# Kernel tuning notes

Measured on AMD Instinct MI355X. Metric: run time of the kernel, lower is better.

The kernel has to match this reference:

```python
import jax, jax.numpy as jnp
import numpy as np

ALPHA = 0.05
MAX_ITER = 200
TOL = 0.01
N = 64
M = 1
BATCH = 262144


def setup_inputs() -> dict:
    key = jax.random.key(0)
    pred_cost = jax.random.normal(key, (BATCH, N), dtype=jnp.float32)
    # constraint data (fixed buffers, match init_kwargs)
    A = np.ones((M, N), dtype=np.float32)
    b = np.full((M,), 32.0, dtype=np.float32)
    lb = np.zeros((N,), dtype=np.float32)
    ub = np.ones((N,), dtype=np.float32)
    # SVD-based pseudoinverse factors for equality projection
    U, s, VT = np.linalg.svd(A, full_matrices=False)
    s_inv = np.where(s >= 1e-6, 1.0 / s, 0.0).astype(np.float32)
    return {
        "pred_cost": pred_cost,
        "A": jnp.asarray(A),
        "b": jnp.asarray(b),
        "lb": jnp.asarray(lb),
        "ub": jnp.asarray(ub),
        "V": jnp.asarray(VT.T.astype(np.float32)),   # (n, m)
        "UT": jnp.asarray(U.T.astype(np.float32)),   # (m, m)
        "s_inv": jnp.asarray(s_inv),                 # (m,)
    }


def _project_box(z, lb, ub):
    return jnp.clip(z, lb, ub)


def _project_equality(w, A, b, V, UT, s_inv):
    # w: (B, n). residual r = A w^T - b, correction = V diag(s_inv) U^T r
    r = w @ A.T - b                      # (B, m)
    corr = ((r @ UT.T) * s_inv) @ V.T    # (B, n)
    return w - corr


def _dys_step(z, cost, A, b, lb, ub, V, UT, s_inv):
    x = _project_box(z, lb, ub)
    grad = cost + ALPHA * x              # grad of regularized objective
    y = _project_equality(2.0 * x - z - ALPHA * grad, A, b, V, UT, s_inv)
    return z - x + y


def _run_to_convergence(cost, A, b, lb, ub, V, UT, s_inv):
    lb_safe = jnp.where(jnp.isfinite(lb), lb, 0.0)
    ub_safe = jnp.where(jnp.isfinite(ub), ub, 1.0)
    z0 = jax.random.uniform(jax.random.key(1), cost.shape, dtype=cost.dtype)
    z0 = z0 * (ub_safe - lb_safe) + lb_safe

    def cond(state):
        i, z, diff = state
        return jnp.logical_and(i < MAX_ITER, diff > TOL)

    def body(state):
        i, z, _ = state
        z_new = _dys_step(z, cost, A, b, lb, ub, V, UT, s_inv)
        diff = jnp.max(jnp.linalg.norm(z_new - z, axis=1))
        return (i + 1, z_new, diff)

    _, z, _ = jax.lax.while_loop(cond, body, (jnp.int32(0), z0, jnp.float32(1e30)))
    return z


def reference(pred_cost, A, b, lb, ub, V, UT, s_inv):
    cost = pred_cost  # minimize=True
    # no-grad fixed-point iterations
    z = jax.lax.stop_gradient(
        _run_to_convergence(jax.lax.stop_gradient(cost), A, b, lb, ub, V, UT, s_inv)
    )
    # training branch: one differentiable DYS step (JFB), then box projection
    z = _dys_step(z, cost, A, b, lb, ub, V, UT, s_inv)
    sol = _project_box(z, lb, ub)
    return sol
```

## Files before the change

kernel.cpp:

```cpp
#include <hip/hip_runtime.h>
#include <cstdint>


#ifndef JAX_PARTITIONABLE
#define JAX_PARTITIONABLE 1
#endif

#define BATCHN 262144
#define MAXIT  200

#define PROBE_ROWS 8192
#define RPW_P  4
#define PROBE_WAVES_P (PROBE_ROWS / RPW_P)

#define NWAVES_A 16384

#define RPW_D  16
#define NWAVES_D (BATCHN / RPW_D)

#define K1 0.9975f
#define K2 1.9975f

typedef float v2f __attribute__((ext_vector_type(2)));

__device__ __forceinline__ void tf2x32(uint32_t x0, uint32_t x1,
                                       uint32_t& o0, uint32_t& o1) {
  const uint32_t k0 = 0u, k1 = 1u;
  const uint32_t k2 = 0x1BD11BDAu ^ k0 ^ k1;
  x0 += k0; x1 += k1;
#define TFR(r) { x0 += x1; x1 = (x1 << (r)) | (x1 >> (32 - (r))); x1 ^= x0; }
  TFR(13) TFR(15) TFR(26) TFR(6)   x0 += k1; x1 += k2 + 1u;
  TFR(17) TFR(29) TFR(16) TFR(24)  x0 += k2; x1 += k0 + 2u;
  TFR(13) TFR(15) TFR(26) TFR(6)   x0 += k0; x1 += k1 + 3u;
  TFR(17) TFR(29) TFR(16) TFR(24)  x0 += k1; x1 += k2 + 4u;
  TFR(13) TFR(15) TFR(26) TFR(6)   x0 += k2; x1 += k0 + 5u;
#undef TFR
  o0 = x0; o1 = x1;
}

__device__ __forceinline__ float z0_at(uint32_t f) {
  uint32_t b;
#if JAX_PARTITIONABLE
  uint32_t o0, o1;
  tf2x32(0u, f, o0, o1);
  b = o0 ^ o1;
#else
  const uint32_t H = 8388608u;
  uint32_t lo = (f < H) ? f : (f - H);
  uint32_t o0, o1;
  tf2x32(lo, lo + H, o0, o1);
  b = (f < H) ? o0 : o1;
#endif
  return __uint_as_float((b >> 9) | 0x3f800000u) - 1.0f;
}

template <int CTRL>
__device__ __forceinline__ float dpp_add(float v) {
  int s = __builtin_amdgcn_mov_dpp(__float_as_int(v), CTRL, 0xF, 0xF, true);
  return v + __int_as_float(s);
}

__device__ __forceinline__ float reduce4(float v) {
  v = dpp_add<0xB1>(v);
  v = dpp_add<0x4E>(v);
  return v;
}

template <int CTRL>
__device__ __forceinline__ v2f dpp_addv(v2f v) {
  int sx = __builtin_amdgcn_mov_dpp(__float_as_int(v.x), CTRL, 0xF, 0xF, true);
  int sy = __builtin_amdgcn_mov_dpp(__float_as_int(v.y), CTRL, 0xF, 0xF, true);
  v2f s;
  s.x = __int_as_float(sx);
  s.y = __int_as_float(sy);
  return v + s;
}

__device__ __forceinline__ v2f reduce16v(v2f v) {
  v = dpp_addv<0xB1>(v);
  v = dpp_addv<0x4E>(v);
  v = dpp_addv<0x124>(v);
  v = dpp_addv<0x128>(v);
  return v;
}

__global__ __launch_bounds__(256, 4) void dys_probe(
    const float* __restrict__ cost, int* __restrict__ Tsample) {
  const int lane = threadIdx.x & 63;
  const int wid  = threadIdx.x >> 6;
  const int gw = blockIdx.x * 4 + wid;
  const int base = (gw * RPW_P + (lane >> 4)) * 64 + (lane & 15) * 4;

  const v2f K1p = {K1, K1};
  const float4 cq = *(const float4*)(cost + base);
  v2f nc0, nc1;
  nc0.x = -cq.x; nc0.y = -cq.y; nc1.x = -cq.z; nc1.y = -cq.w;

  const float z0 = z0_at((uint32_t)(base + 0));
  const float z1 = z0_at((uint32_t)(base + 1));
  const float z2 = z0_at((uint32_t)(base + 2));
  const float z3 = z0_at((uint32_t)(base + 3));
  v2f U0, U1;
  U0.x = 20.0f * z0; U0.y = 20.0f * z1;
  U1.x = 20.0f * z2; U1.y = 20.0f * z3;

  v2f zc;
  zc.x = (z0 + z1) + (z2 + z3);
  zc.y = (cq.x + cq.y) + (cq.z + cq.w);
  zc = reduce16v(zc);
  float R   = __builtin_fmaf(0.05f, zc.y, zc.x);
  const float Snc = -zc.y;
  float SU  = 20.0f * zc.x;
  float CC = 0.0f;

  int ib = MAXIT;
  for (int i = 1; i <= MAXIT; ++i) {
    const float Ch = CC + 20.0f;
    v2f sp, q2v = {0.0f, 0.0f};
    v2f m2, un2, d2;
    m2.x = __builtin_amdgcn_fmed3f(U0.x, CC, Ch);
    m2.y = __builtin_amdgcn_fmed3f(U0.y, CC, Ch);
    sp = m2;
    un2 = __builtin_elementwise_fma(K1p, m2, nc0);
    d2 = un2 - U0;
    q2v = __builtin_elementwise_fma(d2, d2, q2v);
    U0 = un2;
    m2.x = __builtin_amdgcn_fmed3f(U1.x, CC, Ch);
    m2.y = __builtin_amdgcn_fmed3f(U1.y, CC, Ch);
    sp += m2;
    un2 = __builtin_elementwise_fma(K1p, m2, nc1);
    d2 = un2 - U1;
    q2v = __builtin_elementwise_fma(d2, d2, q2v);
    U1 = un2;

    v2f red;
    red.x = sp.x + sp.y;
    red.y = q2v.x + q2v.y;
    red = reduce16v(red);
    const float s_ = red.x;
    const float q2 = red.y;

    const float SUn = __builtin_fmaf(K1, s_, Snc);
    const float q1 = SUn - SU;
    SU = SUn;

    const float Sx = 0.05f * __builtin_fmaf(-64.0f, CC, s_);
    const float t_ = __builtin_fmaf(K2, Sx, -R);
    const float corr20 = __builtin_fmaf(t_, 0.3125f, -10.0f);
    R = (R - Sx) + 32.0f;
    const float CCn = __builtin_fmaf(K1, CC, corr20);
    const float dCC = CCn - CC;
    CC = CCn;
    const float a_ = __builtin_fmaf(64.0f, dCC, -2.0f * q1);
    const float ds = __builtin_fmaf(dCC, a_, q2);
    if (__all(ds <= 0.04f)) { ib = i; break; }
  }

  __shared__ int ibs[4];
  if (lane == 0) ibs[wid] = ib;
  __syncthreads();
  if (threadIdx.x == 0) {
    const int m01 = ibs[0] > ibs[1] ? ibs[0] : ibs[1];
    const int m23 = ibs[2] > ibs[3] ? ibs[2] : ibs[3];
    atomicMax(Tsample, m01 > m23 ? m01 : m23);
  }
}


#define P8(X) X(0) X(1) X(2) X(3) X(4) X(5) X(6) X(7)

#define PAIRS4(X) X(0,0,1) X(1,2,3) X(2,4,5) X(3,6,7)

#define DECL_STATE(p) v2f U##p, nc##p;

#define PIN(p) asm("" : "+v"(U##p), "+v"(nc##p));

#define LOADC(k, p0, p1) { \
  const float4 cq = *(const float4*)(cost + base + 4 * (k)); \
  nc##p0.x = -cq.x; nc##p0.y = -cq.y; nc##p1.x = -cq.z; nc##p1.y = -cq.w; }

#define INITU(p) { \
  const float za = z0_at((uint32_t)(base + 2 * (p))); \
  const float zb = z0_at((uint32_t)(base + 2 * (p) + 1)); \
  U##p.x = 20.0f * za; U##p.y = 20.0f * zb; \
  r0 = __builtin_fmaf(-0.05f, nc##p.x, r0 + za); \
  r1 = __builtin_fmaf(-0.05f, nc##p.y, r1 + zb); }

#define FSTEP(p) { v2f m2; \
  m2.x = __builtin_amdgcn_fmed3f(U##p.x, CC, Ch); \
  m2.y = __builtin_amdgcn_fmed3f(U##p.y, CC, Ch); \
  if ((p) & 1) spB += m2; else spA += m2; \
  U##p = __builtin_elementwise_fma(K1p, m2, nc##p); }

#define FAST_ITER() { \
  const float Ch = CC + 20.0f; \
  v2f spA = {0.0f, 0.0f}, spB = {0.0f, 0.0f}; \
  P8(FSTEP) \
  const v2f spc = spA + spB; \
  const float s_ = reduce4(spc.x + spc.y); \
  const float Sx = 0.05f * __builtin_fmaf(-64.0f, CC, s_); \
  const float t_ = __builtin_fmaf(K2, Sx, -R); \
  const float corr20 = __builtin_fmaf(t_, 0.3125f, -10.0f); \
  R = (R - Sx) + 32.0f; \
  CC = __builtin_fmaf(K1, CC, corr20); }

#define CSTEP(p) { v2f m2; \
  m2.x = __builtin_amdgcn_fmed3f(U##p.x, CC, Ch); \
  m2.y = __builtin_amdgcn_fmed3f(U##p.y, CC, Ch); \
  if ((p) & 1) spB += m2; else spA += m2; \
  const v2f un2 = __builtin_elementwise_fma(K1p, m2, nc##p); \
  const v2f d2 = un2 - U##p; \
  q1v += d2; \
  q2v = __builtin_elementwise_fma(d2, d2, q2v); \
  U##p = un2; }

#define CHK_ITER(DS) { \
  const float Ch = CC + 20.0f; \
  v2f spA = {0.0f, 0.0f}, spB = {0.0f, 0.0f}; \
  v2f q1v = {0.0f, 0.0f}, q2v = {0.0f, 0.0f}; \
  P8(CSTEP) \
  const v2f spc = spA + spB; \
  const float s_ = reduce4(spc.x + spc.y); \
  const float Sx = 0.05f * __builtin_fmaf(-64.0f, CC, s_); \
  const float t_ = __builtin_fmaf(K2, Sx, -R); \
  const float corr20 = __builtin_fmaf(t_, 0.3125f, -10.0f); \
  R = (R - Sx) + 32.0f; \
  const float CCn = __builtin_fmaf(K1, CC, corr20); \
  const float dCC = CCn - CC; CC = CCn; \
  const float q1 = reduce4(q1v.x + q1v.y); \
  const float q2 = reduce4(q2v.x + q2v.y); \
  const float a_ = __builtin_fmaf(64.0f, dCC, -2.0f * q1); \
  DS = __builtin_fmaf(dCC, a_, q2); }

#define STZ(k, p0, p1) { float4 zq; \
  zq.x = __builtin_fmaf(0.05f, U##p0.x, -CC05); \
  zq.y = __builtin_fmaf(0.05f, U##p0.y, -CC05); \
  zq.z = __builtin_fmaf(0.05f, U##p1.x, -CC05); \
  zq.w = __builtin_fmaf(0.05f, U##p1.y, -CC05); \
  *(float4*)(zst + base + 4 * (k)) = zq; }

#define LOADZ(k, p0, p1) { \
  const float4 zq = *(const float4*)(zst + base + 4 * (k)); \
  U##p0.x = 20.0f * zq.x; U##p0.y = 20.0f * zq.y; \
  U##p1.x = 20.0f * zq.z; U##p1.y = 20.0f * zq.w; \
  r0 += zq.x + zq.y; r1 += zq.z + zq.w; }

#define RC(p) { r0 = __builtin_fmaf(-0.05f, nc##p.x, r0); \
  r1 = __builtin_fmaf(-0.05f, nc##p.y, r1); }

#define STOUT(k, p0, p1) { float4 o; \
  o.x = __builtin_amdgcn_fmed3f( \
      __builtin_fmaf(0.05f, U##p0.x, -CC05), 0.0f, 1.0f); \
  o.y = __builtin_amdgcn_fmed3f( \
      __builtin_fmaf(0.05f, U##p0.y, -CC05), 0.0f, 1.0f); \
  o.z = __builtin_amdgcn_fmed3f( \
      __builtin_fmaf(0.05f, U##p1.x, -CC05), 0.0f, 1.0f); \
  o.w = __builtin_amdgcn_fmed3f( \
      __builtin_fmaf(0.05f, U##p1.y, -CC05), 0.0f, 1.0f); \
  *(float4*)(out + base + 4 * (k)) = o; }

__global__ __attribute__((amdgpu_flat_work_group_size(256, 256),
                          amdgpu_waves_per_eu(4, 8)))
void dys_pass1(
    const float* __restrict__ cost, const int* __restrict__ Tsample,
    int* __restrict__ Tglob, int* __restrict__ TrArr,
    float* __restrict__ zst) {
  const int lane = threadIdx.x & 63;
  const int gw = blockIdx.x * 4 + (threadIdx.x >> 6);
  const int base = (gw * RPW_D + (lane >> 2)) * 64 + (lane & 3) * 16;

  const v2f K1p = {K1, K1};
  P8(DECL_STATE)
  PAIRS4(LOADC)
  float r0 = 0.0f, r1 = 0.0f;
  P8(INITU)
  P8(PIN)
  float R = reduce4(r0 + r1);
  float CC = 0.0f;

  const int Ts = *Tsample;
  const int Pn = (Ts > 2) ? (Ts - 2) : 0;

  for (int i = 0; i < Pn; ++i) FAST_ITER();

  int ib = MAXIT;
  for (int i = Pn + 1; i <= MAXIT; ++i) {
    float ds;
    CHK_ITER(ds)
    if (__all(ds <= 0.04f)) { ib = i; break; }
  }

  const float CC05 = 0.05f * CC;
  PAIRS4(STZ)
  if (lane == 0) {
    TrArr[gw] = ib;
    atomicMax(Tglob, ib);
  }
}

__global__ __attribute__((amdgpu_flat_work_group_size(256, 256),
                          amdgpu_waves_per_eu(4, 8)))
void dys_pass2(
    const float* __restrict__ cost, const int* __restrict__ Tglob,
    const int* __restrict__ TrArr, const float* __restrict__ zst,
    float* __restrict__ out) {
  const int lane = threadIdx.x & 63;
  const int gw = blockIdx.x * 4 + (threadIdx.x >> 6);
  const int base = (gw * RPW_D + (lane >> 2)) * 64 + (lane & 3) * 16;

  const v2f K1p = {K1, K1};
  P8(DECL_STATE)
  PAIRS4(LOADC)
  float r0 = 0.0f, r1 = 0.0f;
  PAIRS4(LOADZ)
  P8(RC)
  P8(PIN)
  float R = reduce4(r0 + r1);
  float CC = 0.0f;

  const int T = *Tglob;
  const int ib = TrArr[gw];

  for (int i = ib; i <= T; ++i) FAST_ITER();

  const float CC05 = 0.05f * CC;
  PAIRS4(STOUT)
}

extern "C" void kernel_launch(void* const* d_in, const int* in_sizes, int n_in,
                              void* d_out, int out_size, void* d_ws,
                              size_t ws_size, hipStream_t stream) {
  const float* cost = (const float*)d_in[0];
  float* out = (float*)d_out;

  int* Tglob   = (int*)d_ws;
  int* Tsample = (int*)d_ws + 1;
  const size_t TR_OFF = 1024;
  const size_t Z_OFF  = TR_OFF + (size_t)NWAVES_A * sizeof(int);
  int*   TrArr = (int*)((char*)d_ws + TR_OFF);
  float* zst   = (float*)((char*)d_ws + Z_OFF);

  hipMemsetAsync(d_ws, 0, 8, stream);

  dim3 block(256);
  dys_probe<<<dim3(PROBE_WAVES_P / 4), block, 0, stream>>>(cost, Tsample);
  dys_pass1<<<dim3(NWAVES_D / 4), block, 0, stream>>>(cost, Tsample, Tglob,
                                                      TrArr, zst);
  dys_pass2<<<dim3(NWAVES_D / 4), block, 0, stream>>>(cost, Tglob, TrArr, zst,
                                                      out);
}
```

Baseline: 368.9 us.

## Fuse two DYS passes into one cooperative kernel with grid sync

Replaces the two-pass scheme (pass1 finds each wave's convergence iteration and stores z, pass2 reruns up to the global max) with a single cooperative kernel. Each wave handles two row groups. The first group's state is spilled to the workspace, the second is kept in registers across a grid-wide sync, and then both are finished to the global iteration count. This removes one kernel launch and the reload of state for half of the rows. In exchange, grid size is halved to fit co-residency, which limits parallelism and raises register pressure. If the cooperative launch fails, the code falls back to the old two-kernel path.

```diff
diff --git a/kernel.cpp b/kernel.cpp
--- a/kernel.cpp
+++ b/kernel.cpp
@@ -1,4 +1,5 @@
 #include <hip/hip_runtime.h>
+#include <hip/hip_cooperative_groups.h>
 #include <cstdint>
 
 
@@ -6,6 +7,8 @@
 #define JAX_PARTITIONABLE 1
 #endif
 
+namespace cg = cooperative_groups;
+
 #define BATCHN 262144
 #define MAXIT  200
 
@@ -17,6 +20,8 @@
 
 #define RPW_D  16
 #define NWAVES_D (BATCHN / RPW_D)
+#define FUSED_WAVES (NWAVES_D / 2)
+#define FUSED_BLOCKS (FUSED_WAVES / 4)
 
 #define K1 0.9975f
 #define K2 1.9975f
@@ -260,6 +265,87 @@
   *(float4*)(out + base + 4 * (k)) = o; }
 
 __global__ __attribute__((amdgpu_flat_work_group_size(256, 256),
+                          amdgpu_waves_per_eu(8, 8)))
+void dys_fused(const float* __restrict__ cost,
+               const int* __restrict__ Tsample,
+               int* __restrict__ Tglob,
+               float* __restrict__ zst,
+               float* __restrict__ out) {
+  const int lane = threadIdx.x & 63;
+  const int gw = blockIdx.x * 4 + (threadIdx.x >> 6);
+  const v2f K1p = {K1, K1};
+
+  const int Ts = *Tsample;
+  const int Pn = (Ts > 2) ? (Ts - 2) : 0;
+
+  int ib0 = MAXIT;
+  {
+    const int base = (gw * RPW_D + (lane >> 2)) * 64 + (lane & 3) * 16;
+    P8(DECL_STATE)
+    PAIRS4(LOADC)
+    float r0 = 0.0f, r1 = 0.0f;
+    P8(INITU)
+    P8(PIN)
+    float R = reduce4(r0 + r1);
+    float CC = 0.0f;
+    for (int i = 0; i < Pn; ++i) FAST_ITER();
+    for (int i = Pn + 1; i <= MAXIT; ++i) {
+      float ds;
+      CHK_ITER(ds)
+      if (__all(ds <= 0.04f)) { ib0 = i; break; }
+    }
+    const float CC05 = 0.05f * CC;
+    PAIRS4(STZ)
+  }
+  if (lane == 0) atomicMax(Tglob, ib0);
+
+  P8(DECL_STATE)
+  float CC = 0.0f, R;
+  int ib1 = MAXIT;
+  {
+    const int base = ((FUSED_WAVES + gw) * RPW_D + (lane >> 2)) * 64 +
+                     (lane & 3) * 16;
+    PAIRS4(LOADC)
+    float r0 = 0.0f, r1 = 0.0f;
+    P8(INITU)
+    P8(PIN)
+    R = reduce4(r0 + r1);
+  }
+  for (int i = 0; i < Pn; ++i) FAST_ITER();
+  for (int i = Pn + 1; i <= MAXIT; ++i) {
+    float ds;
+    CHK_ITER(ds)
+    if (__all(ds <= 0.04f)) { ib1 = i; break; }
+  }
+  if (lane == 0) atomicMax(Tglob, ib1);
+
+  cg::this_grid().sync();
+  const int T = *Tglob;
+
+  for (int i = ib1; i <= T; ++i) FAST_ITER();
+  {
+    const int base = ((FUSED_WAVES + gw) * RPW_D + (lane >> 2)) * 64 +
+                     (lane & 3) * 16;
+    const float CC05 = 0.05f * CC;
+    PAIRS4(STOUT)
+  }
+
+  {
+    const int base = (gw * RPW_D + (lane >> 2)) * 64 + (lane & 3) * 16;
+    PAIRS4(LOADC)
+    float r0 = 0.0f, r1 = 0.0f;
+    PAIRS4(LOADZ)
+    P8(RC)
+    P8(PIN)
+    R = reduce4(r0 + r1);
+    CC = 0.0f;
+    for (int i = ib0; i <= T; ++i) FAST_ITER();
+    const float CC05 = 0.05f * CC;
+    PAIRS4(STOUT)
+  }
+}
+
+__global__ __attribute__((amdgpu_flat_work_group_size(256, 256),
                           amdgpu_waves_per_eu(4, 8)))
 void dys_pass1(
     const float* __restrict__ cost, const int* __restrict__ Tsample,
@@ -344,8 +430,17 @@
 
   dim3 block(256);
   dys_probe<<<dim3(PROBE_WAVES_P / 4), block, 0, stream>>>(cost, Tsample);
-  dys_pass1<<<dim3(NWAVES_D / 4), block, 0, stream>>>(cost, Tsample, Tglob,
-                                                      TrArr, zst);
-  dys_pass2<<<dim3(NWAVES_D / 4), block, 0, stream>>>(cost, Tglob, TrArr, zst,
-                                                      out);
-}
+
+  const int* TsampleC = Tsample;
+  void* kargs[] = {(void*)&cost, (void*)&TsampleC, (void*)&Tglob,
+                   (void*)&zst, (void*)&out};
+  hipError_t ce = hipLaunchCooperativeKernel(
+      (const void*)dys_fused, dim3(FUSED_BLOCKS), block, kargs, 0, stream);
+  if (ce != hipSuccess) {
+    (void)hipGetLastError();
+    dys_pass1<<<dim3(NWAVES_D / 4), block, 0, stream>>>(cost, Tsample, Tglob,
+                                                        TrArr, zst);
+    dys_pass2<<<dim3(NWAVES_D / 4), block, 0, stream>>>(cost, Tglob, TrArr,
+                                                        zst, out);
+  }
+}
```

Result: slower. 517.3 us (+40.3%).
